# Kernel tuning notes

Hardware: AMD Instinct MI355X
Metric: run time of the kernel (lower is better)

Reference implementation:

```python
import jax, jax.numpy as jnp
import numpy as np

POOLSCALE = 4  # HSA: avg-pool kernel/stride = (scale, scale*4)

def _avg_pool(x, kh, kw):
    # kernel == stride and dims divisible -> exact reshape-mean pooling
    B, C, H, W = x.shape
    return x.reshape(B, C, H // kh, kh, W // kw, kw).mean(axis=(3, 5))

def setup_inputs() -> dict:
    key = jax.random.key(0)
    k1, k2, k3 = jax.random.split(key, 3)
    shape = (4, 64, 192, 192)
    return {
        "K": jax.random.normal(k1, shape, dtype=jnp.float32),
        "Q": jax.random.normal(k2, shape, dtype=jnp.float32),
        "V": jax.random.normal(k3, shape, dtype=jnp.float32),
    }

def reference(K, Q, V):
    B, C, H, W = Q.shape
    kh, kw = POOLSCALE, POOLSCALE * 4
    Qp = Q.reshape(B, C, H * W).transpose(0, 2, 1)          # [B, HW, C]
    Kp = _avg_pool(K, kh, kw)                               # [B, C, h, w]
    Kp = Kp.reshape(B, C, -1)                               # [B, C, hw_p]
    Vp = _avg_pool(V, kh, kw).reshape(B, C, -1)             # [B, C, hw_p]
    scores = jnp.einsum('bnc,bcm->bnm', Qp, Kp)             # [B, HW, hw_p]
    attn = jax.nn.softmax(scores, axis=1)                   # softmax over query dim (dim=1), as in torch code
    out = jnp.einsum('bcm,bnm->bcn', Vp, attn)              # V_pie @ attn^T -> [B, C, HW]
    return out.reshape(B, C, H, W)
```

## Files before the change

kernel.cpp:

```cpp
#include <hip/hip_runtime.h>
#include <stdint.h>

#define BB 4
#define CC 64
#define HH 192
#define WW 192
#define HWN (HH*WW)
#define KH 4
#define KW 16
#define PW (WW/KW)
#define MP ((HH/KH)*(WW/KW))
#define MITER (MP/64)
#define NBTOT (HWN/32)
#define NUNIT (HWN/64)
#define NGRP 36
#define SCALE_W 65536.0f
#define INV_SCALE (1.0f/65536.0f)
#define LOG2E 1.44269504088896f

typedef _Float16 half8 __attribute__((ext_vector_type(8)));
typedef float floatx4 __attribute__((ext_vector_type(4)));

static __device__ __forceinline__ void gload16(const void* g, void* l) {
  __builtin_amdgcn_global_load_lds((const __attribute__((address_space(1))) void*)g,
                                   (__attribute__((address_space(3))) void*)l, 16, 0, 0);
}
#define WAITCNT_VM(N) asm volatile("s_waitcnt vmcnt(" #N ")" ::: "memory")

static __device__ __forceinline__ float fexp2(float x) {
#if __has_builtin(__builtin_amdgcn_exp2f)
  return __builtin_amdgcn_exp2f(x);
#else
  return __expf(x * 0.6931471805599453f);
#endif
}


__global__ __launch_bounds__(256) void prep_kernel(
    const float* __restrict__ Kin, const float* __restrict__ Vin,
    const float* __restrict__ Q,
    _Float16* __restrict__ kptF, float* __restrict__ vp,
    _Float16* __restrict__ qF) {
  const int POOL_BLOCKS = (2 * BB * CC * MP) / 256;
  if (blockIdx.x < POOL_BLOCKS) {
    int t = blockIdx.x * 256 + threadIdx.x;
    const int total = BB * CC * MP;
    bool isV = t >= total;
    int idx = isV ? t - total : t;
    int m = idx % MP;
    int c = (idx / MP) % CC;
    int b = idx / (MP * CC);
    int mh = m / PW, mw = m % PW;
    const float* src = (isV ? Vin : Kin) + (((b * CC + c) * HH + mh * KH) * WW + mw * KW);
    float s = 0.f;
#pragma unroll
    for (int r = 0; r < KH; ++r) {
      const float4* row = (const float4*)(src + r * WW);
#pragma unroll
      for (int j = 0; j < KW / 4; ++j) {
        float4 v = row[j];
        s += v.x + v.y + v.z + v.w;
      }
    }
    s *= (1.0f / (KH * KW));
    if (isV) {
      vp[(b * CC + c) * MP + m] = s;
    } else {
      int mi = m >> 6, w = m & 63, mf = w >> 4, l15 = w & 15;
      int ks = c >> 5, lhi = (c >> 3) & 3, e = c & 7;
      int lane = lhi * 16 + l15;
      kptF[((((b * MITER + mi) * 4 + mf) * 2 + ks) * 64 + lane) * 8 + e] =
          (_Float16)(s * LOG2E);
    }
  } else {
    int t = (blockIdx.x - POOL_BLOCKS) * 256 + threadIdx.x;
    int chunk = t >> 6;
    int lane = t & 63;
    int nf = chunk & 1;
    int ks = (chunk >> 1) & 1;
    int idx = chunk >> 2;
    int nb = idx % NBTOT;
    int b = idx / NBTOT;
    int c0 = ks * 32 + (lane >> 4) * 8;
    int n = nb * 32 + nf * 16 + (lane & 15);
    const float* Qb = Q + (b * CC + c0) * HWN + n;
    half8 h;
#pragma unroll
    for (int e = 0; e < 8; ++e) h[e] = (_Float16)Qb[e * HWN];
    *(half8*)(qF + chunk * 512 + lane * 8) = h;
  }
}

__global__ __launch_bounds__(256) void colsum_qf2_kernel(
    const _Float16* __restrict__ qF, const _Float16* __restrict__ kptF,
    float* __restrict__ part) {
  int tid = threadIdx.x;
  int lane = tid & 63;
  int l15 = lane & 15;
  int u = blockIdx.x * 4 + (tid >> 6);
  int b = u / NUNIT;
  int un = u % NUNIT;

  const _Float16* qc = qF + (size_t)((b * NBTOT + un * 2) * 4) * 512 + lane * 8;
  half8 af[2][2][2];
#pragma unroll
  for (int nb = 0; nb < 2; ++nb)
#pragma unroll
    for (int ks = 0; ks < 2; ++ks)
#pragma unroll
      for (int nf = 0; nf < 2; ++nf)
        af[nb][nf][ks] = *(const half8*)(qc + (nb * 4 + ks * 2 + nf) * 512);

  const _Float16* kb = kptF + b * MITER * 8 * 512;
  floatx4 zero = {0.f, 0.f, 0.f, 0.f};
  float* pout = part + (size_t)(b * NUNIT + un) * MP;

#pragma unroll
  for (int mi = 0; mi < MITER; ++mi) {
    half8 bfr[4][2];
#pragma unroll
    for (int mf = 0; mf < 4; ++mf)
#pragma unroll
      for (int ks = 0; ks < 2; ++ks)
        bfr[mf][ks] = *(const half8*)(kb + ((mi * 4 + mf) * 2 + ks) * 512 + lane * 8);

    float s0 = 0.f, s1 = 0.f, s2 = 0.f, s3 = 0.f;
#pragma unroll
    for (int nb = 0; nb < 2; ++nb) {
      floatx4 sacc[2][4];
#pragma unroll
      for (int nf = 0; nf < 2; ++nf)
#pragma unroll
        for (int mf = 0; mf < 4; ++mf) sacc[nf][mf] = zero;
      __builtin_amdgcn_s_setprio(1);
#pragma unroll
      for (int ks = 0; ks < 2; ++ks)
#pragma unroll
        for (int nf = 0; nf < 2; ++nf)
#pragma unroll
          for (int mf = 0; mf < 4; ++mf)
            sacc[nf][mf] = __builtin_amdgcn_mfma_f32_16x16x32_f16(
                af[nb][nf][ks], bfr[mf][ks], sacc[nf][mf], 0, 0, 0);
      __builtin_amdgcn_s_setprio(0);
#pragma unroll
      for (int nf = 0; nf < 2; ++nf)
#pragma unroll
        for (int r = 0; r < 4; ++r) {
          s0 += fexp2(sacc[nf][0][r]);
          s1 += fexp2(sacc[nf][1][r]);
          s2 += fexp2(sacc[nf][2][r]);
          s3 += fexp2(sacc[nf][3][r]);
        }
    }
    s0 += __shfl_xor(s0, 16); s0 += __shfl_xor(s0, 32);
    s1 += __shfl_xor(s1, 16); s1 += __shfl_xor(s1, 32);
    s2 += __shfl_xor(s2, 16); s2 += __shfl_xor(s2, 32);
    s3 += __shfl_xor(s3, 16); s3 += __shfl_xor(s3, 32);
    if (lane < 16) {
      float* p = pout + mi * 64;
      p[0 * 16 + l15] = s0;
      p[1 * 16 + l15] = s1;
      p[2 * 16 + l15] = s2;
      p[3 * 16 + l15] = s3;
    }
  }
}

__global__ __launch_bounds__(576) void colsum_reduceA_kernel(
    const float* __restrict__ part, float* __restrict__ part2) {
  int m = threadIdx.x;
  int g = blockIdx.x;
  int b = blockIdx.y;
  const float* p = part + (size_t)(b * NUNIT + g * 16) * MP + m;
  float a0 = 0.f, a1 = 0.f, a2 = 0.f, a3 = 0.f;
#pragma unroll
  for (int j = 0; j < 16; j += 4) {
    a0 += p[(size_t)(j + 0) * MP];
    a1 += p[(size_t)(j + 1) * MP];
    a2 += p[(size_t)(j + 2) * MP];
    a3 += p[(size_t)(j + 3) * MP];
  }
  part2[(size_t)(b * NGRP + g) * MP + m] = (a0 + a1) + (a2 + a3);
}

__global__ __launch_bounds__(256) void colsum_reduceB_kernel(
    const float* __restrict__ part2, float* __restrict__ colsum) {
  int t = blockIdx.x * 256 + threadIdx.x;
  int m = t % MP;
  int b = t / MP;
  const float* p = part2 + (size_t)b * NGRP * MP + m;
  float a0 = 0.f, a1 = 0.f, a2 = 0.f, a3 = 0.f;
#pragma unroll
  for (int g = 0; g < NGRP; g += 4) {
    a0 += p[(size_t)(g + 0) * MP];
    a1 += p[(size_t)(g + 1) * MP];
    a2 += p[(size_t)(g + 2) * MP];
    a3 += p[(size_t)(g + 3) * MP];
  }
  colsum[t] = (a0 + a1) + (a2 + a3);
}

__global__ __launch_bounds__(256) void wprep_kernel(
    const float* __restrict__ vp, const float* __restrict__ colsum,
    _Float16* __restrict__ wqF) {
  int t = blockIdx.x * 256 + threadIdx.x;
  int m = t % MP;
  int c = (t / MP) % CC;
  int b = t / (CC * MP);
  float w = vp[t] / colsum[b * MP + m] * SCALE_W;
  int cf = c >> 4, l15 = c & 15;
  int mi = m >> 6, wl = m & 63;
  int ks = wl >> 5, v = wl & 31;
  int lhi = (v & 15) >> 2;
  int e = (v >> 4) * 4 + (v & 3);
  int lane = lhi * 16 + l15;
  wqF[((((b * MITER + mi) * 4 + cf) * 2 + ks) * 64 + lane) * 8 + e] = (_Float16)w;
}

__global__ __launch_bounds__(256) void attn_v5_kernel(
    const _Float16* __restrict__ qF, const _Float16* __restrict__ kptF,
    const _Float16* __restrict__ wqF, float* __restrict__ out) {
  __shared__ char stg[3 * 16384];
  int b = blockIdx.y;
  int tid = threadIdx.x;
  int wv = tid >> 6;
  int lane = tid & 63;
  int l15 = lane & 15, lhi = lane >> 4;

  const _Float16* kb = kptF + b * MITER * 8 * 512;
  const _Float16* wb = wqF + b * MITER * 8 * 512;

#define STAGE_V5(tt, ss)                                                       \
  {                                                                            \
    int q0_ = wv * 4;                                                          \
    _Pragma("unroll") for (int j_ = 0; j_ < 4; ++j_) {                         \
      int q_ = q0_ + j_;                                                       \
      const _Float16* sp_ = (q_ < 8 ? kb + (tt) * 4096 + q_ * 512              \
                                    : wb + (tt) * 4096 + (q_ - 8) * 512) +     \
                            lane * 8;                                          \
      gload16(sp_, stg + (ss) * 16384 + q_ * 1024);                            \
    }                                                                          \
  }

  int nb0 = blockIdx.x * 8 + wv * 2;
  const _Float16* qc = qF + (size_t)((b * NBTOT + nb0) * 4) * 512 + lane * 8;
  half8 afrag[2][2][2];
#pragma unroll
  for (int j = 0; j < 2; ++j)
#pragma unroll
    for (int ks = 0; ks < 2; ++ks)
#pragma unroll
      for (int nf = 0; nf < 2; ++nf)
        afrag[j][nf][ks] = *(const half8*)(qc + (j * 4 + ks * 2 + nf) * 512);
  STAGE_V5(0, 0);
  STAGE_V5(1, 1);

  floatx4 zero = {0.f, 0.f, 0.f, 0.f};
  floatx4 oacc[2][4][2];
#pragma unroll
  for (int j = 0; j < 2; ++j)
#pragma unroll
    for (int cf = 0; cf < 4; ++cf)
#pragma unroll
      for (int nf = 0; nf < 2; ++nf) oacc[j][cf][nf] = zero;

#pragma unroll
  for (int mi = 0; mi < MITER; ++mi) {
    const int sc = mi % 3;
    if (mi < MITER - 1) { WAITCNT_VM(4); } else { WAITCNT_VM(0); }
    __builtin_amdgcn_sched_barrier(0);
    __builtin_amdgcn_s_barrier();
    if (mi + 2 < MITER) STAGE_V5(mi + 2, (mi + 2) % 3);

    half8 bfr[4][2];
#pragma unroll
    for (int mf = 0; mf < 4; ++mf)
#pragma unroll
      for (int ks = 0; ks < 2; ++ks)
        bfr[mf][ks] = *(const half8*)(stg + sc * 16384 + (mf * 2 + ks) * 1024 + lane * 16);
    half8 wfr[4][2];
#pragma unroll
    for (int cf = 0; cf < 4; ++cf)
#pragma unroll
      for (int ks = 0; ks < 2; ++ks)
        wfr[cf][ks] = *(const half8*)(stg + sc * 16384 + 8192 + (cf * 2 + ks) * 1024 + lane * 16);

#pragma unroll
    for (int j = 0; j < 2; ++j) {
      floatx4 sacc[4][2];
#pragma unroll
      for (int mf = 0; mf < 4; ++mf)
#pragma unroll
        for (int nf = 0; nf < 2; ++nf) sacc[mf][nf] = zero;
      __builtin_amdgcn_s_setprio(1);
#pragma unroll
      for (int ks = 0; ks < 2; ++ks)
#pragma unroll
        for (int mf = 0; mf < 4; ++mf)
#pragma unroll
          for (int nf = 0; nf < 2; ++nf)
            sacc[mf][nf] = __builtin_amdgcn_mfma_f32_16x16x32_f16(
                bfr[mf][ks], afrag[j][nf][ks], sacc[mf][nf], 0, 0, 0);
      __builtin_amdgcn_s_setprio(0);

#pragma unroll
      for (int ks = 0; ks < 2; ++ks) {
        half8 ef[2];
#pragma unroll
        for (int nf = 0; nf < 2; ++nf)
#pragma unroll
          for (int e = 0; e < 8; ++e)
            ef[nf][e] = (_Float16)fexp2(sacc[2 * ks + (e >> 2)][nf][e & 3]);
        __builtin_amdgcn_s_setprio(1);
#pragma unroll
        for (int cf = 0; cf < 4; ++cf)
#pragma unroll
          for (int nf = 0; nf < 2; ++nf)
            oacc[j][cf][nf] = __builtin_amdgcn_mfma_f32_16x16x32_f16(
                wfr[cf][ks], ef[nf], oacc[j][cf][nf], 0, 0, 0);
        __builtin_amdgcn_s_setprio(0);
      }
    }
  }

  float* ob = out + b * CC * HWN;
#pragma unroll
  for (int j = 0; j < 2; ++j)
#pragma unroll
    for (int cf = 0; cf < 4; ++cf)
#pragma unroll
      for (int nf = 0; nf < 2; ++nf)
#pragma unroll
        for (int r = 0; r < 4; ++r) {
          int c = cf * 16 + lhi * 4 + r;
          int n = (nb0 + j) * 32 + nf * 16 + l15;
          ob[c * HWN + n] = oacc[j][cf][nf][r] * INV_SCALE;
        }
}

extern "C" void kernel_launch(void* const* d_in, const int* in_sizes, int n_in,
                              void* d_out, int out_size, void* d_ws, size_t ws_size,
                              hipStream_t stream) {
  const float* K = (const float*)d_in[0];
  const float* Q = (const float*)d_in[1];
  const float* V = (const float*)d_in[2];
  float* out = (float*)d_out;
  char* ws = (char*)d_ws;
  _Float16* kptF  = (_Float16*)(ws);
  float*    vp    = (float*)(ws + 294912);
  _Float16* wqF   = (_Float16*)(ws + 294912 + 589824);
  float*    colsum = (float*)(ws + 294912 + 589824 + 294912);
  const size_t QF_OFF = 1204224;
  _Float16* qF = (_Float16*)(ws + QF_OFF);
  float* part  = out;
  float* part2 = out + 2097152;

  const int POOL_BLOCKS = (2 * BB * CC * MP) / 256;
  const int QPREP_BLOCKS = (BB * NBTOT * 4 * 64) / 256;
  prep_kernel<<<POOL_BLOCKS + QPREP_BLOCKS, 256, 0, stream>>>(K, V, Q, kptF, vp, qF);
  colsum_qf2_kernel<<<(BB * NUNIT) / 4, 256, 0, stream>>>(qF, kptF, part);
  colsum_reduceA_kernel<<<dim3(NGRP, BB), 576, 0, stream>>>(part, part2);
  colsum_reduceB_kernel<<<(BB * MP) / 256, 256, 0, stream>>>(part2, colsum);
  wprep_kernel<<<(BB * CC * MP) / 256, 256, 0, stream>>>(vp, colsum, wqF);
  attn_v5_kernel<<<dim3(NBTOT / 8, BB), 256, 0, stream>>>(qF, kptF, wqF, out);
}
```

Baseline: 82.42 us.

## Restructure prep kernel with LDS-staged coalesced pooling and Q transpose

Rewrites the prep kernel so each block pools an entire (b,c) plane of K and V. It reads the plane fully coalesced as float4, partially sums each float4 into shared memory, then finishes the 4x16 window sums from LDS. Q packing is also changed: a 64-channel by 256-position tile is loaded coalesced, converted to fp16 in padded LDS, then read transposed to build the MFMA fragment layout. This targets the strided per-thread global reads of the old version. The cost is fewer, heavier blocks for pooling (256 blocks) plus extra LDS traffic and barriers.

```diff
diff --git a/kernel.cpp b/kernel.cpp
--- a/kernel.cpp
+++ b/kernel.cpp
@@ -14,11 +14,13 @@
 #define NBTOT (HWN/32)
 #define NUNIT (HWN/64)
 #define NGRP 36
+#define NT256 (HWN/256)
 #define SCALE_W 65536.0f
 #define INV_SCALE (1.0f/65536.0f)
 #define LOG2E 1.44269504088896f
 
 typedef _Float16 half8 __attribute__((ext_vector_type(8)));
+typedef _Float16 half4 __attribute__((ext_vector_type(4)));
 typedef float floatx4 __attribute__((ext_vector_type(4)));
 
 static __device__ __forceinline__ void gload16(const void* g, void* l) {
@@ -36,58 +38,96 @@
 }
 
 
-__global__ __launch_bounds__(256) void prep_kernel(
+__global__ __launch_bounds__(256) void prep2_kernel(
     const float* __restrict__ Kin, const float* __restrict__ Vin,
     const float* __restrict__ Q,
     _Float16* __restrict__ kptF, float* __restrict__ vp,
     _Float16* __restrict__ qF) {
-  const int POOL_BLOCKS = (2 * BB * CC * MP) / 256;
-  if (blockIdx.x < POOL_BLOCKS) {
-    int t = blockIdx.x * 256 + threadIdx.x;
-    const int total = BB * CC * MP;
-    bool isV = t >= total;
-    int idx = isV ? t - total : t;
-    int m = idx % MP;
-    int c = (idx / MP) % CC;
-    int b = idx / (MP * CC);
-    int mh = m / PW, mw = m % PW;
-    const float* src = (isV ? Vin : Kin) + (((b * CC + c) * HH + mh * KH) * WW + mw * KW);
-    float s = 0.f;
-#pragma unroll
-    for (int r = 0; r < KH; ++r) {
-      const float4* row = (const float4*)(src + r * WW);
-#pragma unroll
-      for (int j = 0; j < KW / 4; ++j) {
-        float4 v = row[j];
-        s += v.x + v.y + v.z + v.w;
+  __shared__ float lsf[9216];
+  int tid = threadIdx.x;
+  if (blockIdx.x < BB * CC) {
+    int bc = blockIdx.x;
+    int b = bc / CC, c = bc % CC;
+    int ks = c >> 5, lhi = (c >> 3) & 3, e = c & 7;
+    {
+      const float4* kp4 = (const float4*)(Kin + (size_t)bc * HWN);
+#pragma unroll
+      for (int it = 0; it < 36; ++it) {
+        int idx = it * 256 + tid;
+        float4 v = kp4[idx];
+        lsf[idx] = v.x + v.y + v.z + v.w;
       }
-    }
-    s *= (1.0f / (KH * KW));
-    if (isV) {
-      vp[(b * CC + c) * MP + m] = s;
-    } else {
-      int mi = m >> 6, w = m & 63, mf = w >> 4, l15 = w & 15;
-      int ks = c >> 5, lhi = (c >> 3) & 3, e = c & 7;
-      int lane = lhi * 16 + l15;
-      kptF[((((b * MITER + mi) * 4 + mf) * 2 + ks) * 64 + lane) * 8 + e] =
-          (_Float16)(s * LOG2E);
+      __syncthreads();
+      for (int ci = tid; ci < MP; ci += 256) {
+        int ph = ci / 12, pw = ci % 12;
+        float s = 0.f;
+#pragma unroll
+        for (int r = 0; r < 4; ++r)
+#pragma unroll
+          for (int q = 0; q < 4; ++q)
+            s += lsf[(ph * 4 + r) * 48 + pw * 4 + q];
+        s *= (1.0f / 64.0f);
+        int mi = ci >> 6, w = ci & 63, mf = w >> 4, l15 = w & 15;
+        int lane = lhi * 16 + l15;
+        kptF[((((b * MITER + mi) * 4 + mf) * 2 + ks) * 64 + lane) * 8 + e] =
+            (_Float16)(s * LOG2E);
+      }
+      __syncthreads();
+    }
+    {
+      const float4* vp4 = (const float4*)(Vin + (size_t)bc * HWN);
+#pragma unroll
+      for (int it = 0; it < 36; ++it) {
+        int idx = it * 256 + tid;
+        float4 v = vp4[idx];
+        lsf[idx] = v.x + v.y + v.z + v.w;
+      }
+      __syncthreads();
+      for (int ci = tid; ci < MP; ci += 256) {
+        int ph = ci / 12, pw = ci % 12;
+        float s = 0.f;
+#pragma unroll
+        for (int r = 0; r < 4; ++r)
+#pragma unroll
+          for (int q = 0; q < 4; ++q)
+            s += lsf[(ph * 4 + r) * 48 + pw * 4 + q];
+        vp[(size_t)bc * MP + ci] = s * (1.0f / 64.0f);
+      }
     }
   } else {
-    int t = (blockIdx.x - POOL_BLOCKS) * 256 + threadIdx.x;
-    int chunk = t >> 6;
-    int lane = t & 63;
-    int nf = chunk & 1;
-    int ks = (chunk >> 1) & 1;
-    int idx = chunk >> 2;
-    int nb = idx % NBTOT;
-    int b = idx / NBTOT;
-    int c0 = ks * 32 + (lane >> 4) * 8;
-    int n = nb * 32 + nf * 16 + (lane & 15);
-    const float* Qb = Q + (b * CC + c0) * HWN + n;
-    half8 h;
-#pragma unroll
-    for (int e = 0; e < 8; ++e) h[e] = (_Float16)Qb[e * HWN];
-    *(half8*)(qF + chunk * 512 + lane * 8) = h;
+    int qb = blockIdx.x - BB * CC;
+    int b = qb / NT256, nt = qb % NT256;
+    int n0 = nt * 256;
+    unsigned short* lsu = (unsigned short*)lsf;
+#pragma unroll
+    for (int it = 0; it < 16; ++it) {
+      int idx = it * 256 + tid;
+      int c = idx >> 6, nn = idx & 63;
+      float4 v = *((const float4*)(Q + (size_t)(b * CC + c) * HWN + n0) + nn);
+      half4 hh = {(_Float16)v.x, (_Float16)v.y, (_Float16)v.z, (_Float16)v.w};
+      *(half4*)(&lsu[c * 260 + nn * 4]) = hh;
+    }
+    __syncthreads();
+    int lane = tid & 63, wv = tid >> 6;
+    int l15 = lane & 15, lhi = lane >> 4;
+#pragma unroll
+    for (int nbl2 = 0; nbl2 < 2; ++nbl2) {
+      int nbl = wv * 2 + nbl2;
+      int nb = nt * 8 + nbl;
+#pragma unroll
+      for (int ks = 0; ks < 2; ++ks)
+#pragma unroll
+        for (int nf = 0; nf < 2; ++nf) {
+          int nl = nbl * 32 + nf * 16 + l15;
+          int c0 = ks * 32 + lhi * 8;
+          half8 h;
+#pragma unroll
+          for (int e = 0; e < 8; ++e)
+            h[e] = *(const _Float16*)&lsu[(c0 + e) * 260 + nl];
+          *(half8*)(qF + (size_t)((b * NBTOT + nb) * 4 + ks * 2 + nf) * 512 +
+                    lane * 8) = h;
+        }
+    }
   }
 }
 
@@ -355,9 +395,7 @@
   float* part  = out;
   float* part2 = out + 2097152;
 
-  const int POOL_BLOCKS = (2 * BB * CC * MP) / 256;
-  const int QPREP_BLOCKS = (BB * NBTOT * 4 * 64) / 256;
-  prep_kernel<<<POOL_BLOCKS + QPREP_BLOCKS, 256, 0, stream>>>(K, V, Q, kptF, vp, qF);
+  prep2_kernel<<<BB * CC + BB * NT256, 256, 0, stream>>>(K, V, Q, kptF, vp, qF);
   colsum_qf2_kernel<<<(BB * NUNIT) / 4, 256, 0, stream>>>(qF, kptF, part);
   colsum_reduceA_kernel<<<dim3(NGRP, BB), 576, 0, stream>>>(part, part2);
   colsum_reduceB_kernel<<<(BB * MP) / 256, 256, 0, stream>>>(part2, colsum);
```

Measured after the change: 82.45 us. Within noise of the previous version (+0.0%).

## Restructure prep kernel: split pooling across thread pairs, stage Q transpose through LDS

Applied to the files above, without the earlier changes.

The pooling stage now assigns two threads per pooled cell, each summing two rows and combining the halves with a lane shuffle, which doubles parallelism and shortens per-thread load chains. The Q fp16 repack now loads a 64-channel by 64-position tile into shared memory using direct global-to-LDS loads and transposes it from there. Previously each thread did eight strided scalar global reads. This is meant to make the Q reads coalesced and raise memory-level parallelism. The cost is 16KB of LDS per block and a block barrier, plus LDS reads that may hit bank conflicts.

```diff
diff --git a/kernel.cpp b/kernel.cpp
--- a/kernel.cpp
+++ b/kernel.cpp
@@ -25,6 +25,10 @@
   __builtin_amdgcn_global_load_lds((const __attribute__((address_space(1))) void*)g,
                                    (__attribute__((address_space(3))) void*)l, 16, 0, 0);
 }
+static __device__ __forceinline__ void gload4(const void* g, void* l) {
+  __builtin_amdgcn_global_load_lds((const __attribute__((address_space(1))) void*)g,
+                                   (__attribute__((address_space(3))) void*)l, 4, 0, 0);
+}
 #define WAITCNT_VM(N) asm volatile("s_waitcnt vmcnt(" #N ")" ::: "memory")
 
 static __device__ __forceinline__ float fexp2(float x) {
@@ -36,58 +40,78 @@
 }
 
 
-__global__ __launch_bounds__(256) void prep_kernel(
+#define POOL4_BLOCKS 2304
+#define QPREP4_BLOCKS 2304
+
+__global__ __launch_bounds__(256) void prep4_kernel(
     const float* __restrict__ Kin, const float* __restrict__ Vin,
     const float* __restrict__ Q,
     _Float16* __restrict__ kptF, float* __restrict__ vp,
     _Float16* __restrict__ qF) {
-  const int POOL_BLOCKS = (2 * BB * CC * MP) / 256;
-  if (blockIdx.x < POOL_BLOCKS) {
-    int t = blockIdx.x * 256 + threadIdx.x;
+  __shared__ float lsf[4096];
+  int tid = threadIdx.x;
+  if (blockIdx.x < POOL4_BLOCKS) {
+    int t = blockIdx.x * 256 + tid;
+    int half = t & 1;
+    int rest = t >> 1;
     const int total = BB * CC * MP;
-    bool isV = t >= total;
-    int idx = isV ? t - total : t;
-    int m = idx % MP;
-    int c = (idx / MP) % CC;
-    int b = idx / (MP * CC);
+    bool isV = rest >= total;
+    int cell = isV ? rest - total : rest;
+    int m = cell % MP;
+    int c = (cell / MP) % CC;
+    int b = cell / (MP * CC);
     int mh = m / PW, mw = m % PW;
-    const float* src = (isV ? Vin : Kin) + (((b * CC + c) * HH + mh * KH) * WW + mw * KW);
+    const float* src = (isV ? Vin : Kin) +
+        (((size_t)(b * CC + c) * HH + mh * KH + half * 2) * WW + mw * KW);
     float s = 0.f;
 #pragma unroll
-    for (int r = 0; r < KH; ++r) {
-      const float4* row = (const float4*)(src + r * WW);
-#pragma unroll
-      for (int j = 0; j < KW / 4; ++j) {
-        float4 v = row[j];
-        s += v.x + v.y + v.z + v.w;
+    for (int r = 0; r < 2; ++r) {
+      const floatx4* row = (const floatx4*)(src + r * WW);
+#pragma unroll
+      for (int j = 0; j < 4; ++j) {
+        floatx4 v = row[j];
+        s += (v[0] + v[1]) + (v[2] + v[3]);
       }
     }
-    s *= (1.0f / (KH * KW));
-    if (isV) {
-      vp[(b * CC + c) * MP + m] = s;
-    } else {
-      int mi = m >> 6, w = m & 63, mf = w >> 4, l15 = w & 15;
-      int ks = c >> 5, lhi = (c >> 3) & 3, e = c & 7;
-      int lane = lhi * 16 + l15;
-      kptF[((((b * MITER + mi) * 4 + mf) * 2 + ks) * 64 + lane) * 8 + e] =
-          (_Float16)(s * LOG2E);
+    s += __shfl_xor(s, 1);
+    if (half == 0) {
+      s *= (1.0f / 64.0f);
+      if (isV) {
+        vp[(size_t)(b * CC + c) * MP + m] = s;
+      } else {
+        int mi = m >> 6, w = m & 63, mf = w >> 4, l15 = w & 15;
+        int ks = c >> 5, lhi = (c >> 3) & 3, e = c & 7;
+        int lane = lhi * 16 + l15;
+        kptF[((((b * MITER + mi) * 4 + mf) * 2 + ks) * 64 + lane) * 8 + e] =
+            (_Float16)(s * LOG2E);
+      }
     }
   } else {
-    int t = (blockIdx.x - POOL_BLOCKS) * 256 + threadIdx.x;
-    int chunk = t >> 6;
-    int lane = t & 63;
-    int nf = chunk & 1;
-    int ks = (chunk >> 1) & 1;
-    int idx = chunk >> 2;
-    int nb = idx % NBTOT;
-    int b = idx / NBTOT;
-    int c0 = ks * 32 + (lane >> 4) * 8;
-    int n = nb * 32 + nf * 16 + (lane & 15);
-    const float* Qb = Q + (b * CC + c0) * HWN + n;
-    half8 h;
-#pragma unroll
-    for (int e = 0; e < 8; ++e) h[e] = (_Float16)Qb[e * HWN];
-    *(half8*)(qF + chunk * 512 + lane * 8) = h;
+    int qb = blockIdx.x - POOL4_BLOCKS;
+    int b = qb / NUNIT, t64 = qb % NUNIT;
+    int n0 = t64 * 64;
+    int lane = tid & 63, wv = tid >> 6;
+    int l15 = lane & 15, lhi = lane >> 4;
+#pragma unroll
+    for (int j = 0; j < 16; ++j) {
+      int r = wv * 16 + j;
+      gload4(Q + (size_t)(b * CC + r) * HWN + n0 + lane, lsf + r * 64);
+    }
+    __syncthreads();
+#pragma unroll
+    for (int chh = 0; chh < 2; ++chh) {
+      int ch = wv * 2 + chh;
+      int nbl = ch >> 2, ks = (ch >> 1) & 1, nf = ch & 1;
+      int nb = t64 * 2 + nbl;
+      int nl = nbl * 32 + nf * 16 + l15;
+      int c0 = ks * 32 + lhi * 8;
+      half8 h;
+#pragma unroll
+      for (int e = 0; e < 8; ++e)
+        h[e] = (_Float16)lsf[(c0 + e) * 64 + nl];
+      *(half8*)(qF + (size_t)((b * NBTOT + nb) * 4 + ks * 2 + nf) * 512 +
+                lane * 8) = h;
+    }
   }
 }
 
@@ -355,9 +379,7 @@
   float* part  = out;
   float* part2 = out + 2097152;
 
-  const int POOL_BLOCKS = (2 * BB * CC * MP) / 256;
-  const int QPREP_BLOCKS = (BB * NBTOT * 4 * 64) / 256;
-  prep_kernel<<<POOL_BLOCKS + QPREP_BLOCKS, 256, 0, stream>>>(K, V, Q, kptF, vp, qF);
+  prep4_kernel<<<POOL4_BLOCKS + QPREP4_BLOCKS, 256, 0, stream>>>(K, V, Q, kptF, vp, qF);
   colsum_qf2_kernel<<<(BB * NUNIT) / 4, 256, 0, stream>>>(qF, kptF, part);
   colsum_reduceA_kernel<<<dim3(NGRP, BB), 576, 0, stream>>>(part, part2);
   colsum_reduceB_kernel<<<(BB * MP) / 256, 256, 0, stream>>>(part2, colsum);
```

Measured after the change: 83.06 us. No clear change (+0.8%).
